# Kernel tuning notes

Hardware: AMD Instinct MI355X
Metric: run time of the kernel (lower is better)

The kernel has to match this reference:

```python
import jax, jax.numpy as jnp
import numpy as np

# Model dims
B, T, E, H = 2, 2048, 512, 8
HEAD_DIM = E // H            # 64
NUM_SCALES = 4               # Gauss-Laguerre quadrature nodes
NUM_PRF = 16                 # positive random features per scale
POLY_DIM = 16                # degree-2 TensorSketch dim
EPS = 1e-5
CHUNK = 128                  # chunk size for exact chunked causal linear attention


def setup_inputs() -> dict:
    key = jax.random.key(0)
    ks = jax.random.split(key, 10)
    x = jax.random.normal(ks[0], (B, T, E), jnp.float32)
    sc = 1.0 / np.sqrt(E)  # xavier-ish scale for square projections
    Wq = jax.random.normal(ks[1], (E, E), jnp.float32) * sc
    Wk = jax.random.normal(ks[2], (E, E), jnp.float32) * sc
    Wv = jax.random.normal(ks[3], (E, E), jnp.float32) * sc
    Wo = jax.random.normal(ks[4], (E, E), jnp.float32) * sc
    # FAVOR+ gaussian projections, one block per quadrature scale
    projections = jax.random.normal(ks[5], (NUM_SCALES, NUM_PRF, HEAD_DIM), jnp.float32)
    # Gauss-Laguerre nodes/weights for 1/(C - 2 q.k) = int_0^inf exp(-t(C - 2 q.k)) dt
    nodes, weights = np.polynomial.laguerre.laggauss(NUM_SCALES)
    coef = weights * np.exp(nodes) * np.exp(-nodes * EPS)
    scales = jnp.asarray(np.stack([nodes, coef], axis=1), jnp.float32)  # [S, 2] = (t_s, c_s)
    # degree-2 TensorSketch (count-sketch hashes + rademacher signs)
    sketch_h = jax.random.randint(ks[6], (2, HEAD_DIM), 0, POLY_DIM)
    sketch_s = (jax.random.randint(ks[7], (2, HEAD_DIM), 0, 2) * 2 - 1).astype(jnp.float32)
    return dict(x=x, Wq=Wq, Wk=Wk, Wv=Wv, Wo=Wo, projections=projections,
                scales=scales, sketch_h=sketch_h, sketch_s=sketch_s)


def _features(u, projections, scales, sketch_h, sketch_s):
    """Multi-scale FAVOR+ x TensorSketch feature map for the spherical YAT kernel.

    u: [B,T,H,d], unit-normalized along d. Returns [B,T,H, P*S*m].
    Phi(q).Phi(k) ~= (q.k)^2 / (||q-k||^2 + eps).
    """
    t = scales[:, 0]  # quadrature nodes t_s
    c = scales[:, 1]  # quadrature coeffs w_s e^{t_s} e^{-t_s eps}
    S, m, d = projections.shape
    z = jnp.einsum('smd,bthd->bthsm', projections, u)
    # exp(2 t q.k) via positive RFs; extra e^{-t||u||^2}=e^{-t} (unit sphere) folded in -> -2t
    ef = jnp.exp(jnp.sqrt(2.0 * t)[:, None] * z - 2.0 * t[:, None]) * jnp.sqrt(c / m)[:, None]  # [B,T,H,S,m]
    # degree-2 TensorSketch: countsketch via one-hot matmul, combine with FFT conv
    M1 = sketch_s[0][:, None] * jax.nn.one_hot(sketch_h[0], POLY_DIM, dtype=u.dtype)  # [d,P]
    M2 = sketch_s[1][:, None] * jax.nn.one_hot(sketch_h[1], POLY_DIM, dtype=u.dtype)
    ts = jnp.fft.irfft(jnp.fft.rfft(u @ M1) * jnp.fft.rfft(u @ M2), n=POLY_DIM)  # [B,T,H,P]
    Bs, Ts, Hs = u.shape[:3]
    ef = ef.reshape(Bs, Ts, Hs, S * m)
    return (ts[..., :, None] * ef[..., None, :]).reshape(Bs, Ts, Hs, POLY_DIM * S * m)


def reference(x, Wq, Wk, Wv, Wo, projections, scales, sketch_h, sketch_s):
    Bx, Tx, Ex = x.shape
    d = HEAD_DIM
    q = (x @ Wq).reshape(Bx, Tx, H, d)
    k = (x @ Wk).reshape(Bx, Tx, H, d)
    v = (x @ Wv).reshape(Bx, Tx, H, d)
    # spherical: project q,k to unit sphere
    qn = q / (jnp.linalg.norm(q, axis=-1, keepdims=True) + 1e-6)
    kn = k / (jnp.linalg.norm(k, axis=-1, keepdims=True) + 1e-6)
    fq = _features(qn, projections, scales, sketch_h, sketch_s)  # [B,T,H,F]
    fk = _features(kn, projections, scales, sketch_h, sketch_s)
    F = fq.shape[-1]
    # exact chunked causal linear attention: O(T) state, no [T,T] matrix
    N = Tx // CHUNK
    fq_ = fq.reshape(Bx, N, CHUNK, H, F)
    fk_ = fk.reshape(Bx, N, CHUNK, H, F)
    v_ = v.reshape(Bx, N, CHUNK, H, d)
    kv = jnp.einsum('bnchf,bnchd->bnhfd', fk_, v_)   # per-chunk sum of phi(k) v^T
    kz = fk_.sum(axis=2)                              # [B,N,H,F]
    kv_prev = jnp.concatenate([jnp.zeros_like(kv[:, :1]), jnp.cumsum(kv, axis=1)[:, :-1]], axis=1)
    kz_prev = jnp.concatenate([jnp.zeros_like(kz[:, :1]), jnp.cumsum(kz, axis=1)[:, :-1]], axis=1)
    num = jnp.einsum('bnchf,bnhfd->bnchd', fq_, kv_prev)
    den = jnp.einsum('bnchf,bnhf->bnch', fq_, kz_prev)
    # intra-chunk causal part
    sc = jnp.einsum('bnchf,bnkhf->bnhck', fq_, fk_)
    mask = jnp.tril(jnp.ones((CHUNK, CHUNK), bool))
    scm = jnp.where(mask, sc, 0.0)
    num = num + jnp.einsum('bnhck,bnkhd->bnchd', scm, v_)
    den = den + jnp.swapaxes(scm.sum(axis=-1), 2, 3)
    out = num / (den[..., None] + EPS)
    out = out.reshape(Bx, Tx, Ex) @ Wo
    return out
```

## Files before the change

### kernel.cpp

```cpp
#include <hip/hip_runtime.h>
#include <math.h>

#define B_ 2
#define T_ 2048
#define E_ 512
#define H_ 8
#define D_ 64
#define NCH 16
#define CH 128
#define EPS_ 1e-5f

__global__ __launch_bounds__(256) void gemm512(const float* __restrict__ A,
                                               const float* __restrict__ W,
                                               float* __restrict__ C) {
  __shared__ float As[16][68];
  __shared__ float Bs[16][68];
  const int tid = threadIdx.x;
  const int tx = tid & 15, ty = tid >> 4;
  const int row0 = blockIdx.x * 64, col0 = blockIdx.y * 64;
  const int lr = tid >> 2, lk = (tid & 3) * 4;
  const int bkr = tid >> 4, bcc = (tid & 15) * 4;
  float acc[4][4] = {};
  for (int k0 = 0; k0 < 512; k0 += 16) {
    float4 a4 = *(const float4*)(A + (size_t)(row0 + lr) * 512 + k0 + lk);
    As[lk + 0][lr] = a4.x; As[lk + 1][lr] = a4.y;
    As[lk + 2][lr] = a4.z; As[lk + 3][lr] = a4.w;
    *(float4*)&Bs[bkr][bcc] = *(const float4*)(W + (size_t)(k0 + bkr) * 512 + col0 + bcc);
    __syncthreads();
#pragma unroll
    for (int kk = 0; kk < 16; ++kk) {
      float4 av = *(const float4*)&As[kk][ty * 4];
      float4 bv = *(const float4*)&Bs[kk][tx * 4];
      float aa[4] = {av.x, av.y, av.z, av.w};
      float bb[4] = {bv.x, bv.y, bv.z, bv.w};
#pragma unroll
      for (int i = 0; i < 4; ++i)
#pragma unroll
        for (int j = 0; j < 4; ++j) acc[i][j] += aa[i] * bb[j];
    }
    __syncthreads();
  }
#pragma unroll
  for (int i = 0; i < 4; ++i) {
    float4 o = make_float4(acc[i][0], acc[i][1], acc[i][2], acc[i][3]);
    *(float4*)(C + (size_t)(row0 + ty * 4 + i) * 512 + col0 + tx * 4) = o;
  }
}

__global__ __launch_bounds__(128) void feat_kernel(
    const float* __restrict__ q, const float* __restrict__ k, const float* __restrict__ v,
    const float* __restrict__ proj, const float* __restrict__ scales,
    const int* __restrict__ sh, const float* __restrict__ ss,
    float* __restrict__ Tq, float* __restrict__ Eq,
    float* __restrict__ Tk, float* __restrict__ Ek, float* __restrict__ vh) {
  __shared__ float pj[64][64];
  __shared__ float sq2t[4], m2t[4], cf[4];
  __shared__ int h1[64], h2[64];
  __shared__ float s1[64], s2[64];
  const int tid = threadIdx.x;
  for (int i = tid; i < 4096; i += 128) pj[i >> 6][i & 63] = proj[i];
  if (tid < 4) {
    float t = scales[tid * 2], c = scales[tid * 2 + 1];
    sq2t[tid] = sqrtf(2.f * t); m2t[tid] = -2.f * t; cf[tid] = sqrtf(c / 16.f);
  }
  if (tid < 64) { h1[tid] = sh[tid]; h2[tid] = sh[64 + tid]; s1[tid] = ss[tid]; s2[tid] = ss[64 + tid]; }
  __syncthreads();
  const int isK = blockIdx.y;
  const int row = blockIdx.x * 128 + tid;
  const int h = row & 7; const int bt = row >> 3;
  const int t = bt & (T_ - 1); const int b = bt >> 11;
  const size_t src = (size_t)bt * 512 + h * 64;
  const size_t orow = (size_t)(b * H_ + h) * T_ + t;
  const float* in = (isK ? k : q) + src;
  float* To = (isK ? Tk : Tq) + orow * 16;
  float* Eo = (isK ? Ek : Eq) + orow * 64;

  float u[64]; float nrm = 0.f;
#pragma unroll
  for (int d = 0; d < 64; ++d) { float xv = in[d]; u[d] = xv; nrm += xv * xv; }
  const float inv = 1.f / (sqrtf(nrm) + 1e-6f);
#pragma unroll
  for (int d = 0; d < 64; ++d) u[d] *= inv;

  float p1[16], p2[16];
#pragma unroll
  for (int j = 0; j < 16; ++j) {
    float a1 = 0.f, a2 = 0.f;
#pragma unroll
    for (int d = 0; d < 64; ++d) {
      a1 += (h1[d] == j ? s1[d] : 0.f) * u[d];
      a2 += (h2[d] == j ? s2[d] : 0.f) * u[d];
    }
    p1[j] = a1; p2[j] = a2;
  }
  float tsv[16];
#pragma unroll
  for (int r = 0; r < 16; ++r) {
    float a = 0.f;
#pragma unroll
    for (int j = 0; j < 16; ++j) a += p1[j] * p2[(r - j) & 15];
    tsv[r] = a;
  }
#pragma unroll
  for (int p = 0; p < 16; ++p) To[p] = tsv[p];

#pragma unroll
  for (int s = 0; s < 4; ++s) {
    const float sq = sq2t[s], mb = m2t[s], c = cf[s];
#pragma unroll
    for (int m = 0; m < 16; ++m) {
      float z = 0.f;
      const float* pr = &pj[s * 16 + m][0];
#pragma unroll
      for (int d = 0; d < 64; ++d) z += pr[d] * u[d];
      Eo[s * 16 + m] = expf(sq * z + mb) * c;
    }
  }

  if (!isK) {
    const size_t bt0 = (size_t)blockIdx.x * 16;
    for (int i = tid; i < 16 * 512; i += 128) {
      const size_t bt2 = bt0 + (i >> 9);
      const int hh = (i >> 6) & 7, dd = i & 63;
      const int t2 = (int)(bt2 & (T_ - 1)); const int b2 = (int)(bt2 >> 11);
      vh[((size_t)(b2 * H_ + hh) * T_ + t2) * 64 + dd] = v[bt0 * 512 + i];
    }
  }
}

__global__ __launch_bounds__(256) void kv_kernel(const float* __restrict__ Tk, const float* __restrict__ Ek,
                                                 const float* __restrict__ vh, float* __restrict__ KV) {
  const int bhn = blockIdx.x;
  const int slice = blockIdx.y;
  __shared__ float tks[128][20];
  __shared__ float eks[128][16];
  __shared__ float vs[128][64];
  const int tid = threadIdx.x;
  const size_t rowbase = (size_t)bhn * 128;
  for (int i = tid; i < 2048; i += 256) tks[i >> 4][i & 15] = Tk[rowbase * 16 + i];
  for (int i = tid; i < 2048; i += 256) { int r = i >> 4, e = i & 15; eks[r][e] = Ek[(rowbase + r) * 64 + slice * 16 + e]; }
  for (int i = tid; i < 2048; i += 256) {
    float4 v4 = *(const float4*)(vh + rowbase * 64 + 4 * i);
    *(float4*)&vs[(4 * i) >> 6][(4 * i) & 63] = v4;
  }
  __syncthreads();
  const int d = tid & 63, er = tid >> 6;
  float acc[4][16] = {};
  for (int c = 0; c < 128; ++c) {
    float4 t0 = *(const float4*)&tks[c][0];
    float4 t1 = *(const float4*)&tks[c][4];
    float4 t2 = *(const float4*)&tks[c][8];
    float4 t3 = *(const float4*)&tks[c][12];
    float tkc[16] = {t0.x, t0.y, t0.z, t0.w, t1.x, t1.y, t1.z, t1.w,
                     t2.x, t2.y, t2.z, t2.w, t3.x, t3.y, t3.z, t3.w};
    float4 e4 = *(const float4*)&eks[c][er * 4];
    const float w = vs[c][d];
    float ai[4] = {e4.x * w, e4.y * w, e4.z * w, e4.w * w};
#pragma unroll
    for (int i = 0; i < 4; ++i)
#pragma unroll
      for (int p = 0; p < 16; ++p) acc[i][p] += tkc[p] * ai[i];
  }
  float* out = KV + (size_t)bhn * 65536;
#pragma unroll
  for (int i = 0; i < 4; ++i)
#pragma unroll
    for (int p = 0; p < 16; ++p)
      out[(size_t)(p * 64 + slice * 16 + er * 4 + i) * 64 + d] = acc[i][p];
}

__global__ __launch_bounds__(256) void kz_kernel(const float* __restrict__ Tk, const float* __restrict__ Ek,
                                                 float* __restrict__ KZ) {
  const int bhn = blockIdx.x;
  __shared__ float tks[128][20];
  __shared__ float eks[128][64];
  const int tid = threadIdx.x;
  const size_t rowbase = (size_t)bhn * 128;
  for (int i = tid; i < 2048; i += 256) tks[i >> 4][i & 15] = Tk[rowbase * 16 + i];
  for (int i = tid; i < 2048; i += 256) {
    float4 v4 = *(const float4*)(Ek + rowbase * 64 + 4 * i);
    *(float4*)&eks[(4 * i) >> 6][(4 * i) & 63] = v4;
  }
  __syncthreads();
  const int e = tid & 63, p0 = (tid >> 6) * 4;
  float a[4] = {};
  for (int c = 0; c < 128; ++c) {
    float4 t4 = *(const float4*)&tks[c][p0];
    const float ek = eks[c][e];
    a[0] += t4.x * ek; a[1] += t4.y * ek; a[2] += t4.z * ek; a[3] += t4.w * ek;
  }
#pragma unroll
  for (int j = 0; j < 4; ++j) KZ[(size_t)bhn * 1024 + (p0 + j) * 64 + e] = a[j];
}

__global__ void cumsum_kernel(float* __restrict__ KV, float* __restrict__ KZ) {
  const size_t idx = (size_t)blockIdx.x * 256 + threadIdx.x;
  const size_t nkv = (size_t)B_ * H_ * 65536;
  if (idx < nkv) {
    const size_t bh = idx >> 16, j = idx & 65535;
    float* p = KV + bh * NCH * 65536 + j;
    float a = 0.f;
#pragma unroll
    for (int n = 0; n < NCH; ++n) { const float t = p[(size_t)n << 16]; p[(size_t)n << 16] = a; a += t; }
  } else {
    const size_t i2 = idx - nkv;
    if (i2 < (size_t)B_ * H_ * 1024) {
      const size_t bh = i2 >> 10, j = i2 & 1023;
      float* p = KZ + bh * NCH * 1024 + j;
      float a = 0.f;
#pragma unroll
      for (int n = 0; n < NCH; ++n) { const float t = p[n << 10]; p[n << 10] = a; a += t; }
    }
  }
}

__global__ __launch_bounds__(256) void intra_kernel(const float* __restrict__ Tq, const float* __restrict__ Eq,
                                                    const float* __restrict__ Tk, const float* __restrict__ Ek,
                                                    const float* __restrict__ vh,
                                                    float* __restrict__ numb, float* __restrict__ den) {
  const int bhn = blockIdx.x;
  const int rh = blockIdx.y;
  __shared__ float tks[128][20];
  __shared__ float eks[128][68];
  __shared__ float vs[128][68];
  const int tid = threadIdx.x;
  const int r = tid >> 2, dg = tid & 3, d0 = dg * 16;
  const int nk = (rh + 1) * 64;
  const size_t chunkbase = (size_t)bhn * 128;
  const size_t myrow = chunkbase + rh * 64 + r;

  for (int i = tid; i < nk * 16; i += 256) tks[i >> 4][i & 15] = Tk[chunkbase * 16 + i];
  for (int i = tid; i < nk * 16; i += 256) {
    float4 e4 = *(const float4*)(Ek + chunkbase * 64 + 4 * i);
    *(float4*)&eks[(4 * i) >> 6][(4 * i) & 63] = e4;
    float4 w4 = *(const float4*)(vh + chunkbase * 64 + 4 * i);
    *(float4*)&vs[(4 * i) >> 6][(4 * i) & 63] = w4;
  }
  float tq[16], eq[64];
#pragma unroll
  for (int pp = 0; pp < 4; ++pp) {
    float4 t4 = *(const float4*)(Tq + myrow * 16 + pp * 4);
    tq[pp * 4 + 0] = t4.x; tq[pp * 4 + 1] = t4.y; tq[pp * 4 + 2] = t4.z; tq[pp * 4 + 3] = t4.w;
  }
#pragma unroll
  for (int ee = 0; ee < 16; ++ee) {
    float4 e4 = *(const float4*)(Eq + myrow * 64 + ee * 4);
    eq[ee * 4 + 0] = e4.x; eq[ee * 4 + 1] = e4.y; eq[ee * 4 + 2] = e4.z; eq[ee * 4 + 3] = e4.w;
  }
  __syncthreads();

  float num[16] = {};
  float dn = 0.f;
  const int kmax = rh * 64 + r;
  for (int kk = 0; kk <= kmax; ++kk) {
    float dT = 0.f, dE = 0.f;
#pragma unroll
    for (int pp = 0; pp < 4; ++pp) {
      float4 t4 = *(const float4*)&tks[kk][pp * 4];
      dT += tq[pp * 4 + 0] * t4.x + tq[pp * 4 + 1] * t4.y + tq[pp * 4 + 2] * t4.z + tq[pp * 4 + 3] * t4.w;
    }
#pragma unroll
    for (int ee = 0; ee < 16; ++ee) {
      float4 e4 = *(const float4*)&eks[kk][ee * 4];
      dE += eq[ee * 4 + 0] * e4.x + eq[ee * 4 + 1] * e4.y + eq[ee * 4 + 2] * e4.z + eq[ee * 4 + 3] * e4.w;
    }
    const float s = dT * dE;
    dn += s;
#pragma unroll
    for (int jj = 0; jj < 4; ++jj) {
      float4 v4 = *(const float4*)&vs[kk][d0 + jj * 4];
      num[jj * 4 + 0] += s * v4.x; num[jj * 4 + 1] += s * v4.y;
      num[jj * 4 + 2] += s * v4.z; num[jj * 4 + 3] += s * v4.w;
    }
  }
#pragma unroll
  for (int jj = 0; jj < 4; ++jj) {
    float4 o = make_float4(num[jj * 4 + 0], num[jj * 4 + 1], num[jj * 4 + 2], num[jj * 4 + 3]);
    *(float4*)(numb + myrow * 64 + d0 + jj * 4) = o;
  }
  if (dg == 0) den[myrow] = dn;
}

__global__ __launch_bounds__(256) void inter_kernel(const float* __restrict__ Tq, const float* __restrict__ Eq,
                                                    const float* __restrict__ KV, const float* __restrict__ KZ,
                                                    const float* __restrict__ numb, const float* __restrict__ den,
                                                    float* __restrict__ att) {
  const int bhn = blockIdx.x;
  const int rh = blockIdx.y;
  const int n = bhn & 15, bh = bhn >> 4;
  const int b = bh >> 3, h = bh & 7;
  __shared__ float tqs[64][17];
  __shared__ float eqs[64][68];
  __shared__ float kvp[64][68];
  __shared__ float kzp[64];
  const int tid = threadIdx.x;
  const int tx = tid & 15, ty = tid >> 4;
  const size_t rowbase = (size_t)bhn * 128 + rh * 64;
  for (int i = tid; i < 1024; i += 256) tqs[i >> 4][i & 15] = Tq[rowbase * 16 + i];
  for (int i = tid; i < 1024; i += 256) {
    float4 v4 = *(const float4*)(Eq + rowbase * 64 + 4 * i);
    *(float4*)&eqs[i >> 4][(i & 15) * 4] = v4;
  }
  const float* kvb = KV + (size_t)bhn * 65536;
  const float* kzb = KZ + (size_t)bhn * 1024;
  float acc[4][4] = {};
  float accd[4] = {};
  for (int p = 0; p < 16; ++p) {
    __syncthreads();
#pragma unroll
    for (int j = 0; j < 4; ++j) {
      const int f = tid + 256 * j;
      float4 v4 = *(const float4*)(kvb + p * 4096 + 4 * f);
      *(float4*)&kvp[f >> 4][(f & 15) * 4] = v4;
    }
    if (tid < 64) kzp[tid] = kzb[p * 64 + tid];
    __syncthreads();
    float tqv[4];
#pragma unroll
    for (int ci = 0; ci < 4; ++ci) tqv[ci] = tqs[ty + 16 * ci][p];
    for (int e0 = 0; e0 < 64; e0 += 4) {
      float4 kz4 = *(const float4*)&kzp[e0];
      float4 kv0 = *(const float4*)&kvp[e0 + 0][tx * 4];
      float4 kv1 = *(const float4*)&kvp[e0 + 1][tx * 4];
      float4 kv2 = *(const float4*)&kvp[e0 + 2][tx * 4];
      float4 kv3 = *(const float4*)&kvp[e0 + 3][tx * 4];
#pragma unroll
      for (int ci = 0; ci < 4; ++ci) {
        float4 eq4 = *(const float4*)&eqs[ty + 16 * ci][e0];
        const float a0 = tqv[ci] * eq4.x, a1 = tqv[ci] * eq4.y;
        const float a2 = tqv[ci] * eq4.z, a3 = tqv[ci] * eq4.w;
        acc[ci][0] += a0 * kv0.x; acc[ci][1] += a0 * kv0.y; acc[ci][2] += a0 * kv0.z; acc[ci][3] += a0 * kv0.w;
        acc[ci][0] += a1 * kv1.x; acc[ci][1] += a1 * kv1.y; acc[ci][2] += a1 * kv1.z; acc[ci][3] += a1 * kv1.w;
        acc[ci][0] += a2 * kv2.x; acc[ci][1] += a2 * kv2.y; acc[ci][2] += a2 * kv2.z; acc[ci][3] += a2 * kv2.w;
        acc[ci][0] += a3 * kv3.x; acc[ci][1] += a3 * kv3.y; acc[ci][2] += a3 * kv3.z; acc[ci][3] += a3 * kv3.w;
        accd[ci] += a0 * kz4.x + a1 * kz4.y + a2 * kz4.z + a3 * kz4.w;
      }
    }
  }
#pragma unroll
  for (int ci = 0; ci < 4; ++ci) {
    const int rloc = ty + 16 * ci;
    const size_t row = rowbase + rloc;
    const int t = n * 128 + rh * 64 + rloc;
    const float invd = 1.f / (den[row] + accd[ci] + EPS_);
    float4 nm = *(const float4*)(numb + row * 64 + tx * 4);
    float4 o;
    o.x = (nm.x + acc[ci][0]) * invd;
    o.y = (nm.y + acc[ci][1]) * invd;
    o.z = (nm.z + acc[ci][2]) * invd;
    o.w = (nm.w + acc[ci][3]) * invd;
    *(float4*)(att + (size_t)(b * T_ + t) * 512 + h * 64 + tx * 4) = o;
  }
}

extern "C" void kernel_launch(void* const* d_in, const int* in_sizes, int n_in,
                              void* d_out, int out_size, void* d_ws, size_t ws_size,
                              hipStream_t stream) {
  const float* x   = (const float*)d_in[0];
  const float* Wq  = (const float*)d_in[1];
  const float* Wk  = (const float*)d_in[2];
  const float* Wv  = (const float*)d_in[3];
  const float* Wo  = (const float*)d_in[4];
  const float* prj = (const float*)d_in[5];
  const float* scl = (const float*)d_in[6];
  const int*   shh = (const int*)d_in[7];
  const float* sss = (const float*)d_in[8];

  float* ws  = (float*)d_ws;
  float* q   = ws;
  float* k   = q + 2097152;
  float* v   = k + 2097152;
  float* Tq  = v + 2097152;
  float* Eq  = Tq + 524288;
  float* Tk  = Eq + 2097152;
  float* Ek  = Tk + 524288;
  float* vh  = Ek + 2097152;
  float* KV  = vh + 2097152;
  float* KZ  = KV + 16777216;
  float* nmb = KZ + 262144;
  float* den = nmb + 2097152;
  float* att = den + 32768;

  dim3 gg(64, 8);
  hipLaunchKernelGGL(gemm512, gg, dim3(256), 0, stream, x, Wq, q);
  hipLaunchKernelGGL(gemm512, gg, dim3(256), 0, stream, x, Wk, k);
  hipLaunchKernelGGL(gemm512, gg, dim3(256), 0, stream, x, Wv, v);
  hipLaunchKernelGGL(feat_kernel, dim3(256, 2), dim3(128), 0, stream,
                     q, k, v, prj, scl, shh, sss, Tq, Eq, Tk, Ek, vh);
  hipLaunchKernelGGL(kv_kernel, dim3(256, 4), dim3(256), 0, stream, Tk, Ek, vh, KV);
  hipLaunchKernelGGL(kz_kernel, dim3(256), dim3(256), 0, stream, Tk, Ek, KZ);
  hipLaunchKernelGGL(cumsum_kernel, dim3(4160), dim3(256), 0, stream, KV, KZ);
  hipLaunchKernelGGL(intra_kernel, dim3(256, 2), dim3(256), 0, stream, Tq, Eq, Tk, Ek, vh, nmb, den);
  hipLaunchKernelGGL(inter_kernel, dim3(256, 2), dim3(256), 0, stream, Tq, Eq, KV, KZ, nmb, den, att);
  hipLaunchKernelGGL(gemm512, gg, dim3(256), 0, stream, att, Wo, (float*)d_out);
}
```

Baseline: 481.0 us.

## Restructure feature kernel as shared-memory tiled GEMM and split out V relayout

The feature kernel, which had one thread per row holding 64 registers and doing scalar dot products, becomes a block-cooperative kernel. Normalized rows and a transposed projection matrix are staged in shared memory, and the count-sketch hashing is turned into a dense 64x32 sketch matrix. Projections and sketch are then computed as a register-tiled GEMM, with two threads per row sharing the tensor-sketch convolution. The V head relayout moves to a separate vectorized kernel, which costs one extra launch but removes the strided scalar copy and lowers register pressure.

```diff
diff --git a/kernel.cpp b/kernel.cpp
--- a/kernel.cpp
+++ b/kernel.cpp
@@ -47,85 +47,145 @@
   }
 }
 
-__global__ __launch_bounds__(128) void feat_kernel(
-    const float* __restrict__ q, const float* __restrict__ k, const float* __restrict__ v,
+__global__ __launch_bounds__(256) void feat_kernel(
+    const float* __restrict__ q, const float* __restrict__ k,
     const float* __restrict__ proj, const float* __restrict__ scales,
     const int* __restrict__ sh, const float* __restrict__ ss,
     float* __restrict__ Tq, float* __restrict__ Eq,
-    float* __restrict__ Tk, float* __restrict__ Ek, float* __restrict__ vh) {
-  __shared__ float pj[64][64];
-  __shared__ float sq2t[4], m2t[4], cf[4];
-  __shared__ int h1[64], h2[64];
-  __shared__ float s1[64], s2[64];
-  const int tid = threadIdx.x;
-  for (int i = tid; i < 4096; i += 128) pj[i >> 6][i & 63] = proj[i];
-  if (tid < 4) {
-    float t = scales[tid * 2], c = scales[tid * 2 + 1];
-    sq2t[tid] = sqrtf(2.f * t); m2t[tid] = -2.f * t; cf[tid] = sqrtf(c / 16.f);
-  }
-  if (tid < 64) { h1[tid] = sh[tid]; h2[tid] = sh[64 + tid]; s1[tid] = ss[tid]; s2[tid] = ss[64 + tid]; }
-  __syncthreads();
+    float* __restrict__ Tk, float* __restrict__ Ek) {
+  __shared__ float Us[128][68];
+  __shared__ float PjT[64][68];
+  __shared__ float MT[64][36];
+  __shared__ float Ps[128][36];
+  __shared__ float csq[64], cmb[64], ccf[64];
+  const int tid = threadIdx.x;
   const int isK = blockIdx.y;
-  const int row = blockIdx.x * 128 + tid;
-  const int h = row & 7; const int bt = row >> 3;
-  const int t = bt & (T_ - 1); const int b = bt >> 11;
-  const size_t src = (size_t)bt * 512 + h * 64;
-  const size_t orow = (size_t)(b * H_ + h) * T_ + t;
-  const float* in = (isK ? k : q) + src;
-  float* To = (isK ? Tk : Tq) + orow * 16;
-  float* Eo = (isK ? Ek : Eq) + orow * 64;
-
-  float u[64]; float nrm = 0.f;
-#pragma unroll
-  for (int d = 0; d < 64; ++d) { float xv = in[d]; u[d] = xv; nrm += xv * xv; }
-  const float inv = 1.f / (sqrtf(nrm) + 1e-6f);
-#pragma unroll
-  for (int d = 0; d < 64; ++d) u[d] *= inv;
-
-  float p1[16], p2[16];
-#pragma unroll
-  for (int j = 0; j < 16; ++j) {
-    float a1 = 0.f, a2 = 0.f;
-#pragma unroll
-    for (int d = 0; d < 64; ++d) {
-      a1 += (h1[d] == j ? s1[d] : 0.f) * u[d];
-      a2 += (h2[d] == j ? s2[d] : 0.f) * u[d];
-    }
-    p1[j] = a1; p2[j] = a2;
-  }
-  float tsv[16];
-#pragma unroll
-  for (int r = 0; r < 16; ++r) {
-    float a = 0.f;
-#pragma unroll
-    for (int j = 0; j < 16; ++j) a += p1[j] * p2[(r - j) & 15];
-    tsv[r] = a;
-  }
-#pragma unroll
-  for (int p = 0; p < 16; ++p) To[p] = tsv[p];
-
-#pragma unroll
-  for (int s = 0; s < 4; ++s) {
-    const float sq = sq2t[s], mb = m2t[s], c = cf[s];
-#pragma unroll
-    for (int m = 0; m < 16; ++m) {
-      float z = 0.f;
-      const float* pr = &pj[s * 16 + m][0];
-#pragma unroll
-      for (int d = 0; d < 64; ++d) z += pr[d] * u[d];
-      Eo[s * 16 + m] = expf(sq * z + mb) * c;
-    }
-  }
-
-  if (!isK) {
-    const size_t bt0 = (size_t)blockIdx.x * 16;
-    for (int i = tid; i < 16 * 512; i += 128) {
-      const size_t bt2 = bt0 + (i >> 9);
-      const int hh = (i >> 6) & 7, dd = i & 63;
-      const int t2 = (int)(bt2 & (T_ - 1)); const int b2 = (int)(bt2 >> 11);
-      vh[((size_t)(b2 * H_ + hh) * T_ + t2) * 64 + dd] = v[bt0 * 512 + i];
-    }
-  }
+  const float* in = (isK ? k : q) + (size_t)blockIdx.x * 8192;
+  float* To = isK ? Tk : Tq;
+  float* Eo = isK ? Ek : Eq;
+
+#pragma unroll
+  for (int j = 0; j < 8; ++j) {
+    const int f = tid + 256 * j;
+    float4 a = *(const float4*)(in + 4 * f);
+    *(float4*)&Us[f >> 4][(f & 15) * 4] = a;
+  }
+  for (int i = tid; i < 4096; i += 256) PjT[i & 63][i >> 6] = proj[i];
+  for (int i = tid; i < 64 * 36; i += 256) (&MT[0][0])[i] = 0.f;
+  __syncthreads();
+
+  if (tid < 64) {
+    MT[tid][sh[tid]] = ss[tid];
+    MT[tid][16 + sh[64 + tid]] = ss[64 + tid];
+  } else if (tid < 128) {
+    const int c = tid - 64;
+    const float t = scales[(c >> 4) * 2], cc = scales[(c >> 4) * 2 + 1];
+    csq[c] = sqrtf(2.f * t); cmb[c] = -2.f * t; ccf[c] = sqrtf(cc / 16.f);
+  }
+  {
+    const int r2 = tid >> 1, hf = tid & 1;
+    float4 tv[8]; float s2 = 0.f;
+#pragma unroll
+    for (int j2 = 0; j2 < 8; ++j2) {
+      tv[j2] = *(const float4*)&Us[r2][hf * 32 + 4 * j2];
+      s2 += tv[j2].x * tv[j2].x + tv[j2].y * tv[j2].y + tv[j2].z * tv[j2].z + tv[j2].w * tv[j2].w;
+    }
+    s2 += __shfl_xor(s2, 1);
+    const float inv = 1.f / (sqrtf(s2) + 1e-6f);
+#pragma unroll
+    for (int j2 = 0; j2 < 8; ++j2) {
+      tv[j2].x *= inv; tv[j2].y *= inv; tv[j2].z *= inv; tv[j2].w *= inv;
+      *(float4*)&Us[r2][hf * 32 + 4 * j2] = tv[j2];
+    }
+  }
+  __syncthreads();
+
+  const int tx = tid & 7, ty = tid >> 3;
+  const int c0 = tx * 8, pc0 = tx * 4;
+  float accz[4][8] = {};
+  float accp[4][4] = {};
+  for (int d0 = 0; d0 < 64; d0 += 4) {
+    float Aar[4][4];
+#pragma unroll
+    for (int i = 0; i < 4; ++i) {
+      float4 a4 = *(const float4*)&Us[ty + 32 * i][d0];
+      Aar[i][0] = a4.x; Aar[i][1] = a4.y; Aar[i][2] = a4.z; Aar[i][3] = a4.w;
+    }
+#pragma unroll
+    for (int dd = 0; dd < 4; ++dd) {
+      float4 bl = *(const float4*)&PjT[d0 + dd][c0];
+      float4 bh = *(const float4*)&PjT[d0 + dd][c0 + 4];
+      float4 bm = *(const float4*)&MT[d0 + dd][pc0];
+      float bb[8] = {bl.x, bl.y, bl.z, bl.w, bh.x, bh.y, bh.z, bh.w};
+      float bp[4] = {bm.x, bm.y, bm.z, bm.w};
+#pragma unroll
+      for (int i = 0; i < 4; ++i) {
+        const float a = Aar[i][dd];
+#pragma unroll
+        for (int j = 0; j < 8; ++j) accz[i][j] += a * bb[j];
+#pragma unroll
+        for (int j = 0; j < 4; ++j) accp[i][j] += a * bp[j];
+      }
+    }
+  }
+
+  float sq8[8], mb8[8], cf8[8];
+#pragma unroll
+  for (int j = 0; j < 8; ++j) { sq8[j] = csq[c0 + j]; mb8[j] = cmb[c0 + j]; cf8[j] = ccf[c0 + j]; }
+  const int bx16 = blockIdx.x * 16;
+#pragma unroll
+  for (int i = 0; i < 4; ++i) {
+    const int r = ty + 32 * i;
+    const int bt = bx16 + (r >> 3);
+    const size_t orow = (size_t)((bt >> 11) * 8 + (r & 7)) * 2048 + (bt & 2047);
+    float e[8];
+#pragma unroll
+    for (int j = 0; j < 8; ++j) e[j] = expf(sq8[j] * accz[i][j] + mb8[j]) * cf8[j];
+    *(float4*)(Eo + orow * 64 + c0) = make_float4(e[0], e[1], e[2], e[3]);
+    *(float4*)(Eo + orow * 64 + c0 + 4) = make_float4(e[4], e[5], e[6], e[7]);
+    *(float4*)&Ps[r][pc0] = make_float4(accp[i][0], accp[i][1], accp[i][2], accp[i][3]);
+  }
+  __syncthreads();
+
+  const int rr = tid >> 1, hf2 = tid & 1;
+  float p1v[16], p2v[16];
+#pragma unroll
+  for (int j4 = 0; j4 < 4; ++j4) {
+    float4 a = *(const float4*)&Ps[rr][j4 * 4];
+    p1v[j4 * 4 + 0] = a.x; p1v[j4 * 4 + 1] = a.y; p1v[j4 * 4 + 2] = a.z; p1v[j4 * 4 + 3] = a.w;
+    float4 b2 = *(const float4*)&Ps[rr][16 + j4 * 4];
+    p2v[j4 * 4 + 0] = b2.x; p2v[j4 * 4 + 1] = b2.y; p2v[j4 * 4 + 2] = b2.z; p2v[j4 * 4 + 3] = b2.w;
+  }
+  const int bt2 = bx16 + (rr >> 3);
+  const size_t orow2 = (size_t)((bt2 >> 11) * 8 + (rr & 7)) * 2048 + (bt2 & 2047);
+  float tout[8];
+  if (hf2 == 0) {
+#pragma unroll
+    for (int r8 = 0; r8 < 8; ++r8) {
+      float a = 0.f;
+#pragma unroll
+      for (int j = 0; j < 16; ++j) a += p1v[j] * p2v[(r8 - j) & 15];
+      tout[r8] = a;
+    }
+  } else {
+#pragma unroll
+    for (int r8 = 0; r8 < 8; ++r8) {
+      float a = 0.f;
+#pragma unroll
+      for (int j = 0; j < 16; ++j) a += p1v[j] * p2v[(8 + r8 - j) & 15];
+      tout[r8] = a;
+    }
+  }
+  *(float4*)(To + orow2 * 16 + hf2 * 8) = make_float4(tout[0], tout[1], tout[2], tout[3]);
+  *(float4*)(To + orow2 * 16 + hf2 * 8 + 4) = make_float4(tout[4], tout[5], tout[6], tout[7]);
+}
+
+__global__ __launch_bounds__(256) void vrelayout(const float* __restrict__ v, float* __restrict__ vh) {
+  const int f = blockIdx.x * 256 + threadIdx.x;
+  float4 a = *(const float4*)(v + 4 * (size_t)f);
+  const int d4 = f & 15, h = (f >> 4) & 7, bt = f >> 7;
+  const size_t orow = (size_t)((bt >> 11) * 8 + h) * 2048 + (bt & 2047);
+  *(float4*)(vh + orow * 64 + d4 * 4) = a;
 }
 
 __global__ __launch_bounds__(256) void kv_kernel(const float* __restrict__ Tk, const float* __restrict__ Ek,
@@ -385,8 +445,9 @@
   hipLaunchKernelGGL(gemm512, gg, dim3(256), 0, stream, x, Wq, q);
   hipLaunchKernelGGL(gemm512, gg, dim3(256), 0, stream, x, Wk, k);
   hipLaunchKernelGGL(gemm512, gg, dim3(256), 0, stream, x, Wv, v);
-  hipLaunchKernelGGL(feat_kernel, dim3(256, 2), dim3(128), 0, stream,
-                     q, k, v, prj, scl, shh, sss, Tq, Eq, Tk, Ek, vh);
+  hipLaunchKernelGGL(feat_kernel, dim3(256, 2), dim3(256), 0, stream,
+                     q, k, prj, scl, shh, sss, Tq, Eq, Tk, Ek);
+  hipLaunchKernelGGL(vrelayout, dim3(2048), dim3(256), 0, stream, v, vh);
   hipLaunchKernelGGL(kv_kernel, dim3(256, 4), dim3(256), 0, stream, Tk, Ek, vh, KV);
   hipLaunchKernelGGL(kz_kernel, dim3(256), dim3(256), 0, stream, Tk, Ek, KZ);
   hipLaunchKernelGGL(cumsum_kernel, dim3(4160), dim3(256), 0, stream, KV, KZ);
```

Result: faster. 406.6 us (-15.5%).
